# Optimization experiments

Hardware: AMD Instinct MI355X
Metric: run time of the kernel (lower is better)

The kernel has to match this reference:

```python
import jax, jax.numpy as jnp
import numpy as np

B, C, A, H, W = 8, 64, 32, 64, 64  # batch, input_nf, atten_nf, height, width

def setup_inputs() -> dict:
    key = jax.random.key(0)
    k = jax.random.split(key, 5)
    scale = 1.0 / np.sqrt(C)
    return {
        "x":  jax.random.normal(k[0], (B, C, H, W), dtype=jnp.float32),
        "Wg": jax.random.uniform(k[1], (A, C), jnp.float32, -scale, scale),  # 1x1 conv kernel
        "bg": jax.random.uniform(k[2], (A,),   jnp.float32, -scale, scale),
        "Wh": jax.random.uniform(k[3], (A, C), jnp.float32, -scale, scale),
        "bh": jax.random.uniform(k[4], (A,),   jnp.float32, -scale, scale),
    }

def reference(x, Wg, bg, Wh, bh):
    b, c, h, w = x.shape
    n = h * w
    xf = x.reshape(b, c, n)                               # [B, C, N]
    g = jnp.einsum('ac,bcn->ban', Wg, xf) + bg[None, :, None]  # 1x1 conv == GEMM
    hq = jnp.einsum('ac,bcn->ban', Wh, xf) + bh[None, :, None]
    scores = jnp.einsum('ban,bam->bnm', g, hq)            # [B, N, N]
    alpha = jax.nn.softmax(scores, axis=2)
    r = jnp.einsum('bnm,bcm->bcn', alpha, xf)             # alpha @ x^T, back to [B,C,N]
    r = r.reshape(b, c, h, w)
    r = r + x  # is_residual=True
    return (jax.nn.relu(r), alpha)
```

## Files before the change

### kernel.cpp

```cpp
#include <hip/hip_runtime.h>
#include <hip/hip_bf16.h>
#include <math.h>

#define NB 8
#define NC 64
#define NA 32
#define NN 4096
#define NWAVE 8

typedef __attribute__((ext_vector_type(8))) short bf16x8;
typedef __attribute__((ext_vector_type(4))) short bf16x4;
typedef __attribute__((ext_vector_type(4))) float f32x4;

#if __has_builtin(__builtin_amdgcn_mfma_f32_16x16x16bf16_1k)
  #define HAVE_MFMA16 1
  #define MFMA16(A,B,C) __builtin_amdgcn_mfma_f32_16x16x16bf16_1k(A,B,C,0,0,0)
#elif __has_builtin(__builtin_amdgcn_mfma_f32_16x16x16_bf16)
  #define HAVE_MFMA16 1
  #define MFMA16(A,B,C) __builtin_amdgcn_mfma_f32_16x16x16_bf16(A,B,C,0,0,0)
#else
  #define HAVE_MFMA16 0
#endif

__device__ inline ushort f2bf(float f) {
  union { float f; unsigned u; } v; v.f = f;
  unsigned r = v.u + 0x7fffu + ((v.u >> 16) & 1u);
  return (ushort)(r >> 16);
}

__device__ inline bf16x8 pack8(const f32x4 a, const f32x4 b) {
  union { ushort us[8]; bf16x8 v; } u;
#pragma unroll
  for (int i = 0; i < 4; ++i) { u.us[i] = f2bf(a[i]); u.us[4 + i] = f2bf(b[i]); }
  return u.v;
}

#if HAVE_MFMA16
__device__ inline bf16x4 pk4(const f32x4 p) {
  union { uint u[2]; bf16x4 v; } t;
  asm("v_cvt_pk_bf16_f32 %0, %1, %2" : "=v"(t.u[0]) : "v"(p[0]), "v"(p[1]));
  asm("v_cvt_pk_bf16_f32 %0, %1, %2" : "=v"(t.u[1]) : "v"(p[2]), "v"(p[3]));
  return t.v;
}
#endif

__global__ __launch_bounds__(256) void prep_kernel(
    const float* __restrict__ x, const float* __restrict__ Wg, const float* __restrict__ bg,
    const float* __restrict__ Wh, const float* __restrict__ bh,
    ushort* __restrict__ gT, ushort* __restrict__ hqT, ushort* __restrict__ xfb2)
{
  __shared__ float wg_s[NA * NC];
  __shared__ float wh_s[NA * NC];
  const int t = threadIdx.x;
  for (int i = t; i < NA * NC; i += 256) { wg_s[i] = Wg[i]; wh_s[i] = Wh[i]; }
  __syncthreads();

  const int gid = blockIdx.x * 256 + t;
  const int b = gid >> 12;
  const int n = gid & (NN - 1);
  const float* xb = x + (size_t)b * NC * NN + n;
  const size_t x2base = (size_t)b * NC * NN + (size_t)(n >> 4) * (NC * 16) + (n & 15);

  float accg[NA], acch[NA];
#pragma unroll
  for (int a = 0; a < NA; ++a) { accg[a] = 0.f; acch[a] = 0.f; }

  for (int c4 = 0; c4 < NC / 4; ++c4) {
    const float xv0 = xb[(size_t)(c4 * 4 + 0) * NN];
    const float xv1 = xb[(size_t)(c4 * 4 + 1) * NN];
    const float xv2 = xb[(size_t)(c4 * 4 + 2) * NN];
    const float xv3 = xb[(size_t)(c4 * 4 + 3) * NN];
    xfb2[x2base + (size_t)(c4 * 4 + 0) * 16] = f2bf(xv0);
    xfb2[x2base + (size_t)(c4 * 4 + 1) * 16] = f2bf(xv1);
    xfb2[x2base + (size_t)(c4 * 4 + 2) * 16] = f2bf(xv2);
    xfb2[x2base + (size_t)(c4 * 4 + 3) * 16] = f2bf(xv3);
#pragma unroll
    for (int a = 0; a < NA; ++a) {
      const float4 wg4 = *(const float4*)&wg_s[a * NC + c4 * 4];
      const float4 wh4 = *(const float4*)&wh_s[a * NC + c4 * 4];
      accg[a] += wg4.x * xv0 + wg4.y * xv1 + wg4.z * xv2 + wg4.w * xv3;
      acch[a] += wh4.x * xv0 + wh4.y * xv1 + wh4.z * xv2 + wh4.w * xv3;
    }
  }

  const float LOG2E = 1.44269504088896340736f;
  ushort og[NA], oh[NA];
#pragma unroll
  for (int a = 0; a < NA; ++a) {
    og[a] = f2bf((accg[a] + bg[a]) * LOG2E);
    oh[a] = f2bf(acch[a] + bh[a]);
  }
  const size_t o = ((size_t)b * NN + n) * NA;
#pragma unroll
  for (int k = 0; k < 4; ++k) {
    uint4 vg, vh;
    vg.x = (uint)og[k*8+0] | ((uint)og[k*8+1] << 16);
    vg.y = (uint)og[k*8+2] | ((uint)og[k*8+3] << 16);
    vg.z = (uint)og[k*8+4] | ((uint)og[k*8+5] << 16);
    vg.w = (uint)og[k*8+6] | ((uint)og[k*8+7] << 16);
    vh.x = (uint)oh[k*8+0] | ((uint)oh[k*8+1] << 16);
    vh.y = (uint)oh[k*8+2] | ((uint)oh[k*8+3] << 16);
    vh.z = (uint)oh[k*8+4] | ((uint)oh[k*8+5] << 16);
    vh.w = (uint)oh[k*8+6] | ((uint)oh[k*8+7] << 16);
    *(uint4*)(gT  + o + k * 8) = vg;
    *(uint4*)(hqT + o + k * 8) = vh;
  }
}

__global__ __launch_bounds__(512, 4) void attn_kernel(
    const ushort* __restrict__ gT, const ushort* __restrict__ hqT,
    const ushort* __restrict__ xfb2, const float* __restrict__ x,
    float* __restrict__ outp, float* __restrict__ alpha)
{
  __shared__ float plds[NWAVE][32][32];
  __shared__ float rtile[32][65];
  __shared__ float Lp[NWAVE][32];

  const int tid = threadIdx.x;
  const int l  = tid & 63;
  const int w  = tid >> 6;
  const int lm = l & 15;
  const int lh = l >> 4;

  const int wgid = (blockIdx.x & 7) * 128 + (blockIdx.x >> 3);
  const int b  = wgid >> 7;
  const int n0 = (wgid & 127) << 5;

  const ushort* gB  = gT   + (size_t)b * NN * NA;
  const ushort* hB  = hqT  + (size_t)b * NN * NA;
  const ushort* xB2 = xfb2 + (size_t)b * NC * NN;

  bf16x8 gb0 = *(const bf16x8*)(gB + (size_t)(n0 + lm) * NA + lh * 8);
  bf16x8 gb1 = *(const bf16x8*)(gB + (size_t)(n0 + 16 + lm) * NA + lh * 8);
  const int mbase = w << 9;
  bf16x8 ha0 = *(const bf16x8*)(hB + (size_t)(mbase + lm) * NA + lh * 8);
  bf16x8 ha1 = *(const bf16x8*)(hB + (size_t)(mbase + 16 + lm) * NA + lh * 8);

  float* rflat = &rtile[0][0];
  for (int i = tid; i < 32 * 65; i += 512) rflat[i] = 0.f;

  const f32x4 zz = {0.f, 0.f, 0.f, 0.f};

  float sume0 = 0.f, sume1 = 0.f;
  for (int mc = 0; mc < 16; ++mc) {
    const int m1 = mbase + (((mc + 1) & 15) << 5);
    const bf16x8 na0 = *(const bf16x8*)(hB + (size_t)(m1 + lm) * NA + lh * 8);
    const bf16x8 na1 = *(const bf16x8*)(hB + (size_t)(m1 + 16 + lm) * NA + lh * 8);

    const f32x4 s00 = __builtin_amdgcn_mfma_f32_16x16x32_bf16(ha0, gb0, zz, 0, 0, 0);
    const f32x4 s10 = __builtin_amdgcn_mfma_f32_16x16x32_bf16(ha1, gb0, zz, 0, 0, 0);
    const f32x4 s01 = __builtin_amdgcn_mfma_f32_16x16x32_bf16(ha0, gb1, zz, 0, 0, 0);
    const f32x4 s11 = __builtin_amdgcn_mfma_f32_16x16x32_bf16(ha1, gb1, zz, 0, 0, 0);
#pragma unroll
    for (int r = 0; r < 4; ++r) {
      sume0 += exp2f(s00[r]) + exp2f(s10[r]);
      sume1 += exp2f(s01[r]) + exp2f(s11[r]);
    }
    ha0 = na0; ha1 = na1;
  }
  sume0 += __shfl_xor(sume0, 16); sume0 += __shfl_xor(sume0, 32);
  sume1 += __shfl_xor(sume1, 16); sume1 += __shfl_xor(sume1, 32);
  if (l < 16) { Lp[w][l] = sume0; Lp[w][16 + l] = sume1; }
  __syncthreads();

  float Ls0 = 0.f, Ls1 = 0.f;
#pragma unroll
  for (int ww = 0; ww < NWAVE; ++ww) { Ls0 += Lp[ww][lm]; Ls1 += Lp[ww][16 + lm]; }
  const float Linv0 = 1.0f / Ls0;
  const float Linv1 = 1.0f / Ls1;

  f32x4 racc[2][4];
#pragma unroll
  for (int gi = 0; gi < 2; ++gi)
#pragma unroll
    for (int ci = 0; ci < 4; ++ci) racc[gi][ci] = zz;

  float* aB = alpha + ((size_t)b * NN + n0) * NN;
  const int k7   = lm & 7;
  const int nrow = l >> 3;
  const int uu   = l & 7;

  for (int mc = 0; mc < 16; ++mc) {
    const int m0 = mbase + (mc << 5);
    const int m1 = mbase + (((mc + 1) & 15) << 5);
    const bf16x8 na0 = *(const bf16x8*)(hB + (size_t)(m1 + lm) * NA + lh * 8);
    const bf16x8 na1 = *(const bf16x8*)(hB + (size_t)(m1 + 16 + lm) * NA + lh * 8);

    const f32x4 s00 = __builtin_amdgcn_mfma_f32_16x16x32_bf16(ha0, gb0, zz, 0, 0, 0);
    const f32x4 s10 = __builtin_amdgcn_mfma_f32_16x16x32_bf16(ha1, gb0, zz, 0, 0, 0);
    const f32x4 s01 = __builtin_amdgcn_mfma_f32_16x16x32_bf16(ha0, gb1, zz, 0, 0, 0);
    const f32x4 s11 = __builtin_amdgcn_mfma_f32_16x16x32_bf16(ha1, gb1, zz, 0, 0, 0);

    f32x4 p00, p10, p01, p11;
#pragma unroll
    for (int r = 0; r < 4; ++r) {
      p00[r] = exp2f(s00[r]) * Linv0;
      p10[r] = exp2f(s10[r]) * Linv0;
      p01[r] = exp2f(s01[r]) * Linv1;
      p11[r] = exp2f(s11[r]) * Linv1;
    }

    *(f32x4*)&plds[w][lm]     [((lh    ) ^ k7) << 2] = p00;
    *(f32x4*)&plds[w][lm]     [((lh + 4) ^ k7) << 2] = p10;
    *(f32x4*)&plds[w][16 + lm][((lh    ) ^ k7) << 2] = p01;
    *(f32x4*)&plds[w][16 + lm][((lh + 4) ^ k7) << 2] = p11;

#pragma unroll
    for (int j = 0; j < 4; ++j) {
      const int row = j * 8 + nrow;
      const f32x4 pv = *(const f32x4*)&plds[w][row][(uu ^ (row & 7)) << 2];
      __builtin_nontemporal_store(pv, (f32x4*)(aB + (size_t)row * NN + m0 + uu * 4));
    }

    const int t0 = m0 >> 4;
#if HAVE_MFMA16
    const bf16x4 A00 = pk4(p00);
    const bf16x4 A01 = pk4(p10);
    const bf16x4 A10 = pk4(p01);
    const bf16x4 A11 = pk4(p11);
#pragma unroll
    for (int ci = 0; ci < 4; ++ci) {
      const bf16x4 xv0 = *(const bf16x4*)(xB2 + (size_t)t0       * (NC * 16) + (ci * 16 + lm) * 16 + lh * 4);
      const bf16x4 xv1 = *(const bf16x4*)(xB2 + (size_t)(t0 + 1) * (NC * 16) + (ci * 16 + lm) * 16 + lh * 4);
      racc[0][ci] = MFMA16(A00, xv0, racc[0][ci]);
      racc[0][ci] = MFMA16(A01, xv1, racc[0][ci]);
      racc[1][ci] = MFMA16(A10, xv0, racc[1][ci]);
      racc[1][ci] = MFMA16(A11, xv1, racc[1][ci]);
    }
#else
    const f32x4 q00 = *(const f32x4*)&plds[w][lm]     [((2 * lh    ) ^ k7) << 2];
    const f32x4 q01 = *(const f32x4*)&plds[w][lm]     [((2 * lh + 1) ^ k7) << 2];
    const f32x4 q10 = *(const f32x4*)&plds[w][16 + lm][((2 * lh    ) ^ k7) << 2];
    const f32x4 q11 = *(const f32x4*)&plds[w][16 + lm][((2 * lh + 1) ^ k7) << 2];
    const bf16x8 pa0 = pack8(q00, q01);
    const bf16x8 pa1 = pack8(q10, q11);
#pragma unroll
    for (int ci = 0; ci < 4; ++ci) {
      const bf16x8 xv = *(const bf16x8*)(xB2 + (size_t)(t0 + (lh >> 1)) * (NC * 16) + (ci * 16 + lm) * 16 + (lh & 1) * 8);
      racc[0][ci] = __builtin_amdgcn_mfma_f32_16x16x32_bf16(pa0, xv, racc[0][ci], 0, 0, 0);
      racc[1][ci] = __builtin_amdgcn_mfma_f32_16x16x32_bf16(pa1, xv, racc[1][ci], 0, 0, 0);
    }
#endif
    ha0 = na0; ha1 = na1;
  }

#pragma unroll
  for (int gi = 0; gi < 2; ++gi)
#pragma unroll
    for (int ci = 0; ci < 4; ++ci)
#pragma unroll
      for (int r = 0; r < 4; ++r)
        atomicAdd(&rtile[gi * 16 + lh * 4 + r][ci * 16 + lm], racc[gi][ci][r]);
  __syncthreads();

  const int c  = tid >> 3;
  const int j4 = (tid & 7) << 2;
  f32x4 v;
#pragma unroll
  for (int k = 0; k < 4; ++k) v[k] = rtile[j4 + k][c];
  const size_t oo = ((size_t)b * NC + c) * NN + n0 + j4;
  const f32x4 xr = *(const f32x4*)(x + oo);
#pragma unroll
  for (int k = 0; k < 4; ++k) {
    const float t = v[k] + xr[k];
    v[k] = t > 0.f ? t : 0.f;
  }
  __builtin_nontemporal_store(v, (f32x4*)(outp + oo));
}

extern "C" void kernel_launch(void* const* d_in, const int* in_sizes, int n_in,
                              void* d_out, int out_size, void* d_ws, size_t ws_size,
                              hipStream_t stream) {
  const float* x  = (const float*)d_in[0];
  const float* Wg = (const float*)d_in[1];
  const float* bg = (const float*)d_in[2];
  const float* Wh = (const float*)d_in[3];
  const float* bh = (const float*)d_in[4];

  float* outp  = (float*)d_out;
  float* alpha = outp + (size_t)NB * NC * NN;

  ushort* gT   = (ushort*)d_ws;
  ushort* hqT  = gT + (size_t)NB * NN * NA;
  ushort* xfb2 = hqT + (size_t)NB * NN * NA;

  prep_kernel<<<NB * NN / 256, 256, 0, stream>>>(x, Wg, bg, Wh, bh, gT, hqT, xfb2);
  attn_kernel<<<NB * (NN / 32), 512, 0, stream>>>(gT, hqT, xfb2, x, outp, alpha);
}
```

Before: 213.0 us.

## Move unnormalized alpha@x accumulation into first softmax pass, fold normalization into bias

Computes the r = alpha@x MFMA accumulation in the first (row-sum) pass using unnormalized exp values and scales by 1/L at the end. The output tile is written before the second pass, which now only writes alpha. The second pass folds the normalizer into the MFMA accumulator as a -log2(L) bias, removing the per-element multiply. This balances MFMA/x-load work against the alpha store stream. The risk is that bf16 rounding of the unnormalized exponentials changes precision, and the first pass gains register pressure.

```diff
diff --git a/kernel.cpp b/kernel.cpp
--- a/kernel.cpp
+++ b/kernel.cpp
@@ -33,6 +33,13 @@
 #pragma unroll
   for (int i = 0; i < 4; ++i) { u.us[i] = f2bf(a[i]); u.us[4 + i] = f2bf(b[i]); }
   return u.v;
+}
+
+__device__ inline uint2 packbf(const f32x4 p) {
+  uint2 q;
+  q.x = (uint)f2bf(p[0]) | ((uint)f2bf(p[1]) << 16);
+  q.y = (uint)f2bf(p[2]) | ((uint)f2bf(p[3]) << 16);
+  return q;
 }
 
 #if HAVE_MFMA16
@@ -115,6 +122,10 @@
   __shared__ float plds[NWAVE][32][32];
   __shared__ float rtile[32][65];
   __shared__ float Lp[NWAVE][32];
+  __shared__ float LinvS[32];
+#if !HAVE_MFMA16
+  ushort (*pbuf)[32][36] = reinterpret_cast<ushort (*)[32][36]>(&plds[0][0][0]);
+#endif
 
   const int tid = threadIdx.x;
   const int l  = tid & 63;
@@ -140,24 +151,84 @@
   for (int i = tid; i < 32 * 65; i += 512) rflat[i] = 0.f;
 
   const f32x4 zz = {0.f, 0.f, 0.f, 0.f};
+  f32x4 racc[2][4];
+#pragma unroll
+  for (int gi = 0; gi < 2; ++gi)
+#pragma unroll
+    for (int ci = 0; ci < 4; ++ci) racc[gi][ci] = zz;
 
   float sume0 = 0.f, sume1 = 0.f;
   for (int mc = 0; mc < 16; ++mc) {
+    const int m0 = mbase + (mc << 5);
     const int m1 = mbase + (((mc + 1) & 15) << 5);
+    const int t0 = m0 >> 4;
     const bf16x8 na0 = *(const bf16x8*)(hB + (size_t)(m1 + lm) * NA + lh * 8);
     const bf16x8 na1 = *(const bf16x8*)(hB + (size_t)(m1 + 16 + lm) * NA + lh * 8);
+#if HAVE_MFMA16
+    bf16x4 xv0[4], xv1[4];
+#pragma unroll
+    for (int ci = 0; ci < 4; ++ci) {
+      xv0[ci] = *(const bf16x4*)(xB2 + (size_t)t0       * (NC * 16) + (ci * 16 + lm) * 16 + lh * 4);
+      xv1[ci] = *(const bf16x4*)(xB2 + (size_t)(t0 + 1) * (NC * 16) + (ci * 16 + lm) * 16 + lh * 4);
+    }
+#else
+    bf16x8 xv[4];
+#pragma unroll
+    for (int ci = 0; ci < 4; ++ci)
+      xv[ci] = *(const bf16x8*)(xB2 + (size_t)(t0 + (lh >> 1)) * (NC * 16) + (ci * 16 + lm) * 16 + (lh & 1) * 8);
+#endif
 
     const f32x4 s00 = __builtin_amdgcn_mfma_f32_16x16x32_bf16(ha0, gb0, zz, 0, 0, 0);
     const f32x4 s10 = __builtin_amdgcn_mfma_f32_16x16x32_bf16(ha1, gb0, zz, 0, 0, 0);
     const f32x4 s01 = __builtin_amdgcn_mfma_f32_16x16x32_bf16(ha0, gb1, zz, 0, 0, 0);
     const f32x4 s11 = __builtin_amdgcn_mfma_f32_16x16x32_bf16(ha1, gb1, zz, 0, 0, 0);
+
+    f32x4 e00, e10, e01, e11;
 #pragma unroll
     for (int r = 0; r < 4; ++r) {
-      sume0 += exp2f(s00[r]) + exp2f(s10[r]);
-      sume1 += exp2f(s01[r]) + exp2f(s11[r]);
-    }
+      e00[r] = exp2f(s00[r]);
+      e10[r] = exp2f(s10[r]);
+      e01[r] = exp2f(s01[r]);
+      e11[r] = exp2f(s11[r]);
+      sume0 += e00[r] + e10[r];
+      sume1 += e01[r] + e11[r];
+    }
+
+#if HAVE_MFMA16
+    const bf16x4 A00 = pk4(e00);
+    const bf16x4 A01 = pk4(e10);
+    const bf16x4 A10 = pk4(e01);
+    const bf16x4 A11 = pk4(e11);
+#pragma unroll
+    for (int ci = 0; ci < 4; ++ci) {
+      racc[0][ci] = MFMA16(A00, xv0[ci], racc[0][ci]);
+      racc[0][ci] = MFMA16(A01, xv1[ci], racc[0][ci]);
+      racc[1][ci] = MFMA16(A10, xv0[ci], racc[1][ci]);
+      racc[1][ci] = MFMA16(A11, xv1[ci], racc[1][ci]);
+    }
+#else
+    *(uint2*)&pbuf[w][lm][lh * 4]           = packbf(e00);
+    *(uint2*)&pbuf[w][lm][16 + lh * 4]      = packbf(e10);
+    *(uint2*)&pbuf[w][16 + lm][lh * 4]      = packbf(e01);
+    *(uint2*)&pbuf[w][16 + lm][16 + lh * 4] = packbf(e11);
+    union UB { uint4 u; bf16x8 v; } ua, ub;
+    {
+      const uint2 a0 = *(const uint2*)&pbuf[w][lm][lh * 8];
+      const uint2 a1 = *(const uint2*)&pbuf[w][lm][lh * 8 + 4];
+      ua.u = make_uint4(a0.x, a0.y, a1.x, a1.y);
+      const uint2 b0 = *(const uint2*)&pbuf[w][16 + lm][lh * 8];
+      const uint2 b1 = *(const uint2*)&pbuf[w][16 + lm][lh * 8 + 4];
+      ub.u = make_uint4(b0.x, b0.y, b1.x, b1.y);
+    }
+#pragma unroll
+    for (int ci = 0; ci < 4; ++ci) {
+      racc[0][ci] = __builtin_amdgcn_mfma_f32_16x16x32_bf16(ua.v, xv[ci], racc[0][ci], 0, 0, 0);
+      racc[1][ci] = __builtin_amdgcn_mfma_f32_16x16x32_bf16(ub.v, xv[ci], racc[1][ci], 0, 0, 0);
+    }
+#endif
     ha0 = na0; ha1 = na1;
   }
+
   sume0 += __shfl_xor(sume0, 16); sume0 += __shfl_xor(sume0, 32);
   sume1 += __shfl_xor(sume1, 16); sume1 += __shfl_xor(sume1, 32);
   if (l < 16) { Lp[w][l] = sume0; Lp[w][16 + l] = sume1; }
@@ -166,15 +237,43 @@
   float Ls0 = 0.f, Ls1 = 0.f;
 #pragma unroll
   for (int ww = 0; ww < NWAVE; ++ww) { Ls0 += Lp[ww][lm]; Ls1 += Lp[ww][16 + lm]; }
-  const float Linv0 = 1.0f / Ls0;
-  const float Linv1 = 1.0f / Ls1;
-
-  f32x4 racc[2][4];
+  const float blog0 = -log2f(Ls0);
+  const float blog1 = -log2f(Ls1);
+
+  if (tid < 32) {
+    float s = 0.f;
+#pragma unroll
+    for (int ww = 0; ww < NWAVE; ++ww) s += Lp[ww][tid];
+    LinvS[tid] = 1.0f / s;
+  }
+
 #pragma unroll
   for (int gi = 0; gi < 2; ++gi)
 #pragma unroll
-    for (int ci = 0; ci < 4; ++ci) racc[gi][ci] = zz;
-
+    for (int ci = 0; ci < 4; ++ci)
+#pragma unroll
+      for (int r = 0; r < 4; ++r)
+        atomicAdd(&rtile[gi * 16 + lh * 4 + r][ci * 16 + lm], racc[gi][ci][r]);
+  __syncthreads();
+
+  {
+    const int c  = tid >> 3;
+    const int j4 = (tid & 7) << 2;
+    f32x4 v;
+#pragma unroll
+    for (int k = 0; k < 4; ++k) v[k] = rtile[j4 + k][c] * LinvS[j4 + k];
+    const size_t oo = ((size_t)b * NC + c) * NN + n0 + j4;
+    const f32x4 xr = *(const f32x4*)(x + oo);
+#pragma unroll
+    for (int k = 0; k < 4; ++k) {
+      const float t = v[k] + xr[k];
+      v[k] = t > 0.f ? t : 0.f;
+    }
+    __builtin_nontemporal_store(v, (f32x4*)(outp + oo));
+  }
+
+  const f32x4 bias0 = {blog0, blog0, blog0, blog0};
+  const f32x4 bias1 = {blog1, blog1, blog1, blog1};
   float* aB = alpha + ((size_t)b * NN + n0) * NN;
   const int k7   = lm & 7;
   const int nrow = l >> 3;
@@ -186,18 +285,18 @@
     const bf16x8 na0 = *(const bf16x8*)(hB + (size_t)(m1 + lm) * NA + lh * 8);
     const bf16x8 na1 = *(const bf16x8*)(hB + (size_t)(m1 + 16 + lm) * NA + lh * 8);
 
-    const f32x4 s00 = __builtin_amdgcn_mfma_f32_16x16x32_bf16(ha0, gb0, zz, 0, 0, 0);
-    const f32x4 s10 = __builtin_amdgcn_mfma_f32_16x16x32_bf16(ha1, gb0, zz, 0, 0, 0);
-    const f32x4 s01 = __builtin_amdgcn_mfma_f32_16x16x32_bf16(ha0, gb1, zz, 0, 0, 0);
-    const f32x4 s11 = __builtin_amdgcn_mfma_f32_16x16x32_bf16(ha1, gb1, zz, 0, 0, 0);
+    const f32x4 s00 = __builtin_amdgcn_mfma_f32_16x16x32_bf16(ha0, gb0, bias0, 0, 0, 0);
+    const f32x4 s10 = __builtin_amdgcn_mfma_f32_16x16x32_bf16(ha1, gb0, bias0, 0, 0, 0);
+    const f32x4 s01 = __builtin_amdgcn_mfma_f32_16x16x32_bf16(ha0, gb1, bias1, 0, 0, 0);
+    const f32x4 s11 = __builtin_amdgcn_mfma_f32_16x16x32_bf16(ha1, gb1, bias1, 0, 0, 0);
 
     f32x4 p00, p10, p01, p11;
 #pragma unroll
     for (int r = 0; r < 4; ++r) {
-      p00[r] = exp2f(s00[r]) * Linv0;
-      p10[r] = exp2f(s10[r]) * Linv0;
-      p01[r] = exp2f(s01[r]) * Linv1;
-      p11[r] = exp2f(s11[r]) * Linv1;
+      p00[r] = exp2f(s00[r]);
+      p10[r] = exp2f(s10[r]);
+      p01[r] = exp2f(s01[r]);
+      p11[r] = exp2f(s11[r]);
     }
 
     *(f32x4*)&plds[w][lm]     [((lh    ) ^ k7) << 2] = p00;
@@ -211,61 +310,8 @@
       const f32x4 pv = *(const f32x4*)&plds[w][row][(uu ^ (row & 7)) << 2];
       __builtin_nontemporal_store(pv, (f32x4*)(aB + (size_t)row * NN + m0 + uu * 4));
     }
-
-    const int t0 = m0 >> 4;
-#if HAVE_MFMA16
-    const bf16x4 A00 = pk4(p00);
-    const bf16x4 A01 = pk4(p10);
-    const bf16x4 A10 = pk4(p01);
-    const bf16x4 A11 = pk4(p11);
-#pragma unroll
-    for (int ci = 0; ci < 4; ++ci) {
-      const bf16x4 xv0 = *(const bf16x4*)(xB2 + (size_t)t0       * (NC * 16) + (ci * 16 + lm) * 16 + lh * 4);
-      const bf16x4 xv1 = *(const bf16x4*)(xB2 + (size_t)(t0 + 1) * (NC * 16) + (ci * 16 + lm) * 16 + lh * 4);
-      racc[0][ci] = MFMA16(A00, xv0, racc[0][ci]);
-      racc[0][ci] = MFMA16(A01, xv1, racc[0][ci]);
-      racc[1][ci] = MFMA16(A10, xv0, racc[1][ci]);
-      racc[1][ci] = MFMA16(A11, xv1, racc[1][ci]);
-    }
-#else
-    const f32x4 q00 = *(const f32x4*)&plds[w][lm]     [((2 * lh    ) ^ k7) << 2];
-    const f32x4 q01 = *(const f32x4*)&plds[w][lm]     [((2 * lh + 1) ^ k7) << 2];
-    const f32x4 q10 = *(const f32x4*)&plds[w][16 + lm][((2 * lh    ) ^ k7) << 2];
-    const f32x4 q11 = *(const f32x4*)&plds[w][16 + lm][((2 * lh + 1) ^ k7) << 2];
-    const bf16x8 pa0 = pack8(q00, q01);
-    const bf16x8 pa1 = pack8(q10, q11);
-#pragma unroll
-    for (int ci = 0; ci < 4; ++ci) {
-      const bf16x8 xv = *(const bf16x8*)(xB2 + (size_t)(t0 + (lh >> 1)) * (NC * 16) + (ci * 16 + lm) * 16 + (lh & 1) * 8);
-      racc[0][ci] = __builtin_amdgcn_mfma_f32_16x16x32_bf16(pa0, xv, racc[0][ci], 0, 0, 0);
-      racc[1][ci] = __builtin_amdgcn_mfma_f32_16x16x32_bf16(pa1, xv, racc[1][ci], 0, 0, 0);
-    }
-#endif
     ha0 = na0; ha1 = na1;
   }
-
-#pragma unroll
-  for (int gi = 0; gi < 2; ++gi)
-#pragma unroll
-    for (int ci = 0; ci < 4; ++ci)
-#pragma unroll
-      for (int r = 0; r < 4; ++r)
-        atomicAdd(&rtile[gi * 16 + lh * 4 + r][ci * 16 + lm], racc[gi][ci][r]);
-  __syncthreads();
-
-  const int c  = tid >> 3;
-  const int j4 = (tid & 7) << 2;
-  f32x4 v;
-#pragma unroll
-  for (int k = 0; k < 4; ++k) v[k] = rtile[j4 + k][c];
-  const size_t oo = ((size_t)b * NC + c) * NN + n0 + j4;
-  const f32x4 xr = *(const f32x4*)(x + oo);
-#pragma unroll
-  for (int k = 0; k < 4; ++k) {
-    const float t = v[k] + xr[k];
-    v[k] = t > 0.f ? t : 0.f;
-  }
-  __builtin_nontemporal_store(v, (f32x4*)(outp + oo));
 }
 
 extern "C" void kernel_launch(void* const* d_in, const int* in_sizes, int n_in,
```

New measurement: 218.9 us. 1.03x slower.
